# Optimization experiments

Measured on AMD Instinct MI355X. Metric: run time of the kernel, lower is better.

Reference implementation:

```python
import jax, jax.numpy as jnp
import numpy as np

B, S, H, D = 4, 128, 32, 128
T = 2048  # max_seq_len (cache length)
START_POS = 1024


def setup_inputs() -> dict:
    key = jax.random.key(0)
    ks = jax.random.split(key, 5)
    q = jax.random.normal(ks[0], (B, S, H, D), dtype=jnp.float32)
    k = jax.random.normal(ks[1], (B, S, H, D), dtype=jnp.float32)
    v = jax.random.normal(ks[2], (B, S, H, D), dtype=jnp.float32)
    k_cache = jax.random.normal(ks[3], (B, T, H, D), dtype=jnp.float32)
    v_cache = jax.random.normal(ks[4], (B, T, H, D), dtype=jnp.float32)
    return {"q": q, "k": k, "v": v, "k_cache": k_cache, "v_cache": v_cache,
            "input_pos": START_POS, "seq_len": S}


def reference(q, k, v, k_cache, v_cache, input_pos, seq_len):
    # Fused KV-cache append + causal SDPA (llama.sdpa_with_kv_cache semantics).
    # q/k/v: [B, S, H, D]; caches: [B, T, H, D]; input_pos = write offset.
    start = input_pos
    kc = jax.lax.dynamic_update_slice(k_cache, k, (0, start, 0, 0))
    vc = jax.lax.dynamic_update_slice(v_cache, v, (0, start, 0, 0))

    scale = 1.0 / jnp.sqrt(jnp.asarray(q.shape[-1], q.dtype))
    # scores: [B, H, S, T]
    scores = jnp.einsum('bshd,bthd->bhst', q, kc) * scale

    # causal mask relative to absolute positions: query i (global start+i)
    # attends to cache positions j <= start + i
    qpos = start + jnp.arange(seq_len)            # [S]
    kpos = jnp.arange(kc.shape[1])                # [T]
    mask = kpos[None, :] <= qpos[:, None]         # [S, T]
    neg = jnp.asarray(jnp.finfo(scores.dtype).min, scores.dtype)
    scores = jnp.where(mask[None, None], scores, neg)

    attn = jax.nn.softmax(scores, axis=-1)        # dropout = 0.0 (inference)
    out = jnp.einsum('bhst,bthd->bshd', attn, vc)  # [B, S, H, D]
    bsz = q.shape[0]
    return out.reshape(bsz, seq_len, -1)          # [B, S, H*D]
```

## Files before the change

### kernel.cpp

```cpp
#include <hip/hip_runtime.h>
#include <hip/hip_bf16.h>


typedef short bf16x8 __attribute__((ext_vector_type(8)));
typedef float f32x4  __attribute__((ext_vector_type(4)));

constexpr int B = 4, S = 128, H = 32, D = 128, T = 2048;
constexpr int KVBLK = 64;
constexpr int NS = 4;
constexpr float SCALE = 0.08838834764831845f;
constexpr float MNEG = -1e30f;

__device__ __forceinline__ short f2bf(float f) {
    return (short)__bfloat16_as_ushort(__float2bfloat16(f));
}
__device__ __forceinline__ unsigned pack_bf2(float a, float b) {
    return (unsigned)(unsigned short)__bfloat16_as_ushort(__float2bfloat16(a))
         | ((unsigned)__bfloat16_as_ushort(__float2bfloat16(b)) << 16);
}

__device__ __forceinline__ int kswz(int row, int cb) { return row * 256 + (cb ^ ((row & 7) << 4)); }
__device__ __forceinline__ int vswz(int row, int cb) { return 16384 + row * 128 + (cb ^ ((row & 7) << 4)); }

template<int MODE>
__global__ __launch_bounds__(512, 2) void sdpa_kernel(
    const float* __restrict__ qg, const float* __restrict__ kin,
    const float* __restrict__ vin, const float* __restrict__ kc,
    const float* __restrict__ vc, const int* __restrict__ ip,
    float* __restrict__ out, float* __restrict__ wsO, float2* __restrict__ wsML)
{
    __shared__ __align__(16) char smem[32768];

    const int start = ip[0];
    const int bh = blockIdx.x;
    const int b  = bh >> 5;
    const int h  = bh & 31;
    const int z  = (MODE == 1) ? blockIdx.z : 0;
    const int t  = threadIdx.x;
    const int w  = t >> 6;
    const int l  = t & 63;
    const int l16 = l & 15;
    const int lg  = l >> 4;
    const int qi  = w * 16 + l16;

    const float* qp = qg + (((size_t)b * S + qi) * H + h) * D;
    bf16x8 qfrag[4];
    #pragma unroll
    for (int ks = 0; ks < 4; ++ks) {
        const float* p = qp + ks * 32 + lg * 8;
        #pragma unroll
        for (int i = 0; i < 8; ++i) qfrag[ks][i] = f2bf(p[i]);
    }

    f32x4 oaccT[8];
    #pragma unroll
    for (int n = 0; n < 8; ++n) oaccT[n] = {0.f, 0.f, 0.f, 0.f};
    float m = MNEG, ssum = 0.f;

    const int kv_end = start + S;
    const int nt     = (kv_end + KVBLK - 1) / KVBLK;
    const int tstep  = (MODE == 1) ? NS : 1;
    const int t0     = (MODE == 1) ? z : 0;

    const int kr = t >> 5, c = t & 31;
    const int rb = t & 15, cb = t >> 4;

    auto kaddr = [&](int j) -> const float4* {
        return (j < start)
            ? (const float4*)(kc  + (((size_t)b * T + j) * H + h) * (size_t)D)
            : (const float4*)(kin + (((size_t)b * S + (j - start)) * H + h) * (size_t)D);
    };
    auto vaddr = [&](int j) -> const float4* {
        return (j < start)
            ? (const float4*)(vc  + (((size_t)b * T + j) * H + h) * (size_t)D)
            : (const float4*)(vin + (((size_t)b * S + (j - start)) * H + h) * (size_t)D);
    };

    for (int tile = t0; tile < nt; tile += tstep) {
        const int j0 = tile * KVBLK;

        #pragma unroll
        for (int g = 0; g < 2; ++g) {
            float4 kt[2];
            #pragma unroll
            for (int p = 0; p < 2; ++p) kt[p] = kaddr(j0 + (g * 2 + p) * 16 + kr)[c];
            #pragma unroll
            for (int p = 0; p < 2; ++p) {
                short4 k4b = { f2bf(kt[p].x), f2bf(kt[p].y), f2bf(kt[p].z), f2bf(kt[p].w) };
                *(short4*)(smem + kswz((g * 2 + p) * 16 + kr, c * 8)) = k4b;
            }
        }
        {
            float4 a[4];
            #pragma unroll
            for (int kk = 0; kk < 4; ++kk)
                a[kk] = vaddr(j0 + rb * 4 + kk)[cb];
            #pragma unroll
            for (int jj = 0; jj < 4; ++jj) {
                const int d = cb * 4 + jj;
                short4 wv = { f2bf(((const float*)&a[0])[jj]),
                              f2bf(((const float*)&a[1])[jj]),
                              f2bf(((const float*)&a[2])[jj]),
                              f2bf(((const float*)&a[3])[jj]) };
                *(short4*)(smem + vswz(d, rb * 8)) = wv;
            }
        }
        __syncthreads();

        if (j0 <= start + w * 16 + 15) {
            f32x4 sacc[4];
            #pragma unroll
            for (int n = 0; n < 4; ++n) sacc[n] = {0.f, 0.f, 0.f, 0.f};
            #pragma unroll
            for (int n = 0; n < 4; ++n) {
                #pragma unroll
                for (int ks = 0; ks < 4; ++ks) {
                    bf16x8 kfrag = *(const bf16x8*)(smem + kswz(n * 16 + l16, ks * 64 + lg * 16));
                    sacc[n] = __builtin_amdgcn_mfma_f32_16x16x32_bf16(
                        kfrag, qfrag[ks], sacc[n], 0, 0, 0);
                }
            }

            float pmax = MNEG;
            #pragma unroll
            for (int n = 0; n < 4; ++n) {
                #pragma unroll
                for (int j = 0; j < 4; ++j) {
                    const int kvj = j0 + n * 16 + lg * 4 + j;
                    float s = sacc[n][j] * SCALE;
                    if (kvj > start + qi) s = MNEG;
                    sacc[n][j] = s;
                    pmax = fmaxf(pmax, s);
                }
            }
            pmax = fmaxf(pmax, __shfl_xor(pmax, 16));
            pmax = fmaxf(pmax, __shfl_xor(pmax, 32));
            const float mnew = fmaxf(m, pmax);
            const float corr = __expf(m - mnew);
            m = mnew;

            float tsum = 0.f;
            unsigned plo[4], phi[4];
            #pragma unroll
            for (int n = 0; n < 4; ++n) {
                float p0 = __expf(sacc[n][0] - m);
                float p1 = __expf(sacc[n][1] - m);
                float p2 = __expf(sacc[n][2] - m);
                float p3 = __expf(sacc[n][3] - m);
                tsum += (p0 + p1) + (p2 + p3);
                plo[n] = pack_bf2(p0, p1);
                phi[n] = pack_bf2(p2, p3);
            }
            tsum += __shfl_xor(tsum, 16);
            tsum += __shfl_xor(tsum, 32);
            ssum = ssum * corr + tsum;
            #pragma unroll
            for (int n = 0; n < 8; ++n) {
                #pragma unroll
                for (int j = 0; j < 4; ++j) oaccT[n][j] *= corr;
            }

            const int sA = (((2 * lg)     & 3) << 4) | l16;
            const int sB = (((2 * lg + 1) & 3) << 4) | l16;
            const bool hi = (lg >= 2);
            bf16x8 pfragB[2];
            #pragma unroll
            for (int ks = 0; ks < 2; ++ks) {
                unsigned eA0 = __shfl(plo[2 * ks],     sA), eA1 = __shfl(phi[2 * ks],     sA);
                unsigned fA0 = __shfl(plo[2 * ks + 1], sA), fA1 = __shfl(phi[2 * ks + 1], sA);
                unsigned eB0 = __shfl(plo[2 * ks],     sB), eB1 = __shfl(phi[2 * ks],     sB);
                unsigned fB0 = __shfl(plo[2 * ks + 1], sB), fB1 = __shfl(phi[2 * ks + 1], sB);
                union { unsigned u[4]; bf16x8 v; } cv;
                cv.u[0] = hi ? fA0 : eA0;
                cv.u[1] = hi ? fA1 : eA1;
                cv.u[2] = hi ? fB0 : eB0;
                cv.u[3] = hi ? fB1 : eB1;
                pfragB[ks] = cv.v;
            }

            #pragma unroll
            for (int ks = 0; ks < 2; ++ks) {
                #pragma unroll
                for (int n = 0; n < 8; ++n) {
                    bf16x8 vfrag = *(const bf16x8*)(smem + vswz(n * 16 + l16, ks * 64 + lg * 16));
                    oaccT[n] = __builtin_amdgcn_mfma_f32_16x16x32_bf16(
                        vfrag, pfragB[ks], oaccT[n], 0, 0, 0);
                }
            }
        }
        __syncthreads();
    }

    float* scr = (float*)(smem + w * 4096);
    const float inv = (MODE == 0) ? 1.0f / ssum : 1.0f;
    #pragma unroll
    for (int half = 0; half < 2; ++half) {
        #pragma unroll
        for (int n2 = 0; n2 < 4; ++n2) {
            const int n = half * 4 + n2;
            #pragma unroll
            for (int j = 0; j < 4; ++j) {
                const int dl = n2 * 16 + lg * 4 + j;
                scr[l16 * 64 + (((dl & ~3) ^ ((l16 & 7) << 2)) | (dl & 3))] =
                    oaccT[n][j] * inv;
            }
        }
        asm volatile("s_waitcnt lgkmcnt(0)" ::: "memory");
        __builtin_amdgcn_sched_barrier(0);
        #pragma unroll
        for (int pass = 0; pass < 4; ++pass) {
            const int r  = pass * 4 + (l >> 4);
            const int d0 = (l & 15) * 4;
            f32x4 val = *(f32x4*)&scr[r * 64 + (d0 ^ ((r & 7) << 2))];
            const int qr = w * 16 + r;
            const int dc = half * 64 + d0;
            if (MODE == 0) {
                *(f32x4*)(out + ((size_t)b * S + qr) * (size_t)(H * D) + h * D + dc) = val;
            } else {
                *(f32x4*)(wsO + ((((size_t)z * B + b) * S + qr) * H + h) * (size_t)D + dc) = val;
            }
        }
        asm volatile("s_waitcnt lgkmcnt(0)" ::: "memory");
        __builtin_amdgcn_sched_barrier(0);
    }
    if (MODE == 1 && lg == 0)
        wsML[(((size_t)z * B + b) * S + qi) * H + h] = make_float2(m, ssum);
}

__global__ __launch_bounds__(256) void combine_kernel(
    const float* __restrict__ wsO, const float2* __restrict__ wsML,
    float* __restrict__ out)
{
    constexpr int R    = B * S * H;
    constexpr int TOT4 = R * D / 4;
    for (int i4 = blockIdx.x * 256 + threadIdx.x; i4 < TOT4;
         i4 += gridDim.x * 256) {
        const int row = i4 >> 5;
        float2 e[NS];
        float M = MNEG;
        #pragma unroll
        for (int cc = 0; cc < NS; ++cc) {
            e[cc] = wsML[(size_t)cc * R + row];
            M = fmaxf(M, e[cc].x);
        }
        float L = 0.f;
        float v0 = 0.f, v1 = 0.f, v2 = 0.f, v3 = 0.f;
        #pragma unroll
        for (int cc = 0; cc < NS; ++cc) {
            const float wgt = __expf(e[cc].x - M);
            L += e[cc].y * wgt;
            float4 tv = ((const float4*)wsO)[(size_t)cc * TOT4 + i4];
            v0 += tv.x * wgt; v1 += tv.y * wgt; v2 += tv.z * wgt; v3 += tv.w * wgt;
        }
        const float inv = 1.0f / L;
        ((float4*)out)[i4] = make_float4(v0 * inv, v1 * inv, v2 * inv, v3 * inv);
    }
}

extern "C" void kernel_launch(void* const* d_in, const int* in_sizes, int n_in,
                              void* d_out, int out_size, void* d_ws, size_t ws_size,
                              hipStream_t stream) {
    const float* q  = (const float*)d_in[0];
    const float* k  = (const float*)d_in[1];
    const float* v  = (const float*)d_in[2];
    const float* kc = (const float*)d_in[3];
    const float* vc = (const float*)d_in[4];
    const int*   ip = (const int*)d_in[5];
    float* out = (float*)d_out;

    const size_t nO  = (size_t)NS * B * S * H * D;
    const size_t nML = (size_t)NS * B * S * H;
    const size_t need = (nO + 2 * nML) * sizeof(float);

    if (ws_size >= need) {
        float*  wsO  = (float*)d_ws;
        float2* wsML = (float2*)(wsO + nO);
        sdpa_kernel<1><<<dim3(B * H, 1, NS), 512, 0, stream>>>(
            q, k, v, kc, vc, ip, out, wsO, wsML);
        combine_kernel<<<2048, 256, 0, stream>>>(wsO, wsML, out);
    } else {
        sdpa_kernel<0><<<dim3(B * H), 512, 0, stream>>>(
            q, k, v, kc, vc, ip, out, nullptr, nullptr);
    }
}
```

Measured before the change: 45.48 us.

## Double-buffer K/V tiles in LDS and prefetch next tile during compute

Doubles the shared-memory buffer to 64KB and restructures the KV loop into a software pipeline. The next tile's K and V global loads are issued before the current tile's QK and PV MFMAs, and the bf16 conversion and LDS stores go into the alternate buffer, so one barrier per iteration is dropped. The aim is to hide global-memory latency behind compute. The larger LDS footprint (64KB per block with launch_bounds(512,2)) may reduce occupancy, and the prefetched registers add pressure.

Result: slower. 52.73 us (+16.0%).

```diff
diff --git a/kernel.cpp b/kernel.cpp
--- a/kernel.cpp
+++ b/kernel.cpp
@@ -29,7 +29,7 @@
     const float* __restrict__ vc, const int* __restrict__ ip,
     float* __restrict__ out, float* __restrict__ wsO, float2* __restrict__ wsML)
 {
-    __shared__ __align__(16) char smem[32768];
+    __shared__ __align__(16) char smem[65536];
 
     const int start = ip[0];
     const int bh = blockIdx.x;
@@ -76,46 +76,57 @@
             : (const float4*)(vin + (((size_t)b * S + (j - start)) * H + h) * (size_t)D);
     };
 
+    {
+        const int j0 = t0 * KVBLK;
+        #pragma unroll
+        for (int p = 0; p < 4; ++p) {
+            float4 kt = kaddr(j0 + p * 16 + kr)[c];
+            short4 k4b = { f2bf(kt.x), f2bf(kt.y), f2bf(kt.z), f2bf(kt.w) };
+            *(short4*)(smem + kswz(p * 16 + kr, c * 8)) = k4b;
+        }
+        float4 a[4];
+        #pragma unroll
+        for (int kk = 0; kk < 4; ++kk) a[kk] = vaddr(j0 + rb * 4 + kk)[cb];
+        #pragma unroll
+        for (int jj = 0; jj < 4; ++jj) {
+            const int d = cb * 4 + jj;
+            short4 wv = { f2bf(((const float*)&a[0])[jj]),
+                          f2bf(((const float*)&a[1])[jj]),
+                          f2bf(((const float*)&a[2])[jj]),
+                          f2bf(((const float*)&a[3])[jj]) };
+            *(short4*)(smem + vswz(d, rb * 8)) = wv;
+        }
+    }
+    __syncthreads();
+
+    int cur = 0;
     for (int tile = t0; tile < nt; tile += tstep) {
-        const int j0 = tile * KVBLK;
-
-        #pragma unroll
-        for (int g = 0; g < 2; ++g) {
-            float4 kt[2];
-            #pragma unroll
-            for (int p = 0; p < 2; ++p) kt[p] = kaddr(j0 + (g * 2 + p) * 16 + kr)[c];
-            #pragma unroll
-            for (int p = 0; p < 2; ++p) {
-                short4 k4b = { f2bf(kt[p].x), f2bf(kt[p].y), f2bf(kt[p].z), f2bf(kt[p].w) };
-                *(short4*)(smem + kswz((g * 2 + p) * 16 + kr, c * 8)) = k4b;
-            }
-        }
-        {
-            float4 a[4];
-            #pragma unroll
-            for (int kk = 0; kk < 4; ++kk)
-                a[kk] = vaddr(j0 + rb * 4 + kk)[cb];
-            #pragma unroll
-            for (int jj = 0; jj < 4; ++jj) {
-                const int d = cb * 4 + jj;
-                short4 wv = { f2bf(((const float*)&a[0])[jj]),
-                              f2bf(((const float*)&a[1])[jj]),
-                              f2bf(((const float*)&a[2])[jj]),
-                              f2bf(((const float*)&a[3])[jj]) };
-                *(short4*)(smem + vswz(d, rb * 8)) = wv;
-            }
-        }
-        __syncthreads();
-
-        if (j0 <= start + w * 16 + 15) {
-            f32x4 sacc[4];
+        const int j0   = tile * KVBLK;
+        const int nxt  = tile + tstep;
+        const bool pre = (nxt < nt);
+        const int cb_cur = cur << 15;
+        const int cb_nxt = cb_cur ^ 32768;
+        const bool active = (j0 <= start + w * 16 + 15);
+
+        float4 kt[4];
+        if (pre) {
+            const int j0n = nxt * KVBLK;
+            #pragma unroll
+            for (int p = 0; p < 4; ++p) kt[p] = kaddr(j0n + p * 16 + kr)[c];
+        }
+        __builtin_amdgcn_sched_barrier(0);
+
+        f32x4 sacc[4];
+        unsigned plo[4], phi[4];
+        float corr;
+        if (active) {
             #pragma unroll
             for (int n = 0; n < 4; ++n) sacc[n] = {0.f, 0.f, 0.f, 0.f};
             #pragma unroll
             for (int n = 0; n < 4; ++n) {
                 #pragma unroll
                 for (int ks = 0; ks < 4; ++ks) {
-                    bf16x8 kfrag = *(const bf16x8*)(smem + kswz(n * 16 + l16, ks * 64 + lg * 16));
+                    bf16x8 kfrag = *(const bf16x8*)(smem + cb_cur + kswz(n * 16 + l16, ks * 64 + lg * 16));
                     sacc[n] = __builtin_amdgcn_mfma_f32_16x16x32_bf16(
                         kfrag, qfrag[ks], sacc[n], 0, 0, 0);
                 }
@@ -136,11 +147,10 @@
             pmax = fmaxf(pmax, __shfl_xor(pmax, 16));
             pmax = fmaxf(pmax, __shfl_xor(pmax, 32));
             const float mnew = fmaxf(m, pmax);
-            const float corr = __expf(m - mnew);
+            corr = __expf(m - mnew);
             m = mnew;
 
             float tsum = 0.f;
-            unsigned plo[4], phi[4];
             #pragma unroll
             for (int n = 0; n < 4; ++n) {
                 float p0 = __expf(sacc[n][0] - m);
@@ -159,7 +169,25 @@
                 #pragma unroll
                 for (int j = 0; j < 4; ++j) oaccT[n][j] *= corr;
             }
-
+        }
+
+        if (pre) {
+            #pragma unroll
+            for (int p = 0; p < 4; ++p) {
+                short4 k4b = { f2bf(kt[p].x), f2bf(kt[p].y), f2bf(kt[p].z), f2bf(kt[p].w) };
+                *(short4*)(smem + cb_nxt + kswz(p * 16 + kr, c * 8)) = k4b;
+            }
+        }
+
+        float4 av[4];
+        if (pre) {
+            const int j0n = nxt * KVBLK;
+            #pragma unroll
+            for (int kk = 0; kk < 4; ++kk) av[kk] = vaddr(j0n + rb * 4 + kk)[cb];
+        }
+        __builtin_amdgcn_sched_barrier(0);
+
+        if (active) {
             const int sA = (((2 * lg)     & 3) << 4) | l16;
             const int sB = (((2 * lg + 1) & 3) << 4) | l16;
             const bool hi = (lg >= 2);
@@ -182,13 +210,26 @@
             for (int ks = 0; ks < 2; ++ks) {
                 #pragma unroll
                 for (int n = 0; n < 8; ++n) {
-                    bf16x8 vfrag = *(const bf16x8*)(smem + vswz(n * 16 + l16, ks * 64 + lg * 16));
+                    bf16x8 vfrag = *(const bf16x8*)(smem + cb_cur + vswz(n * 16 + l16, ks * 64 + lg * 16));
                     oaccT[n] = __builtin_amdgcn_mfma_f32_16x16x32_bf16(
                         vfrag, pfragB[ks], oaccT[n], 0, 0, 0);
                 }
             }
         }
+
+        if (pre) {
+            #pragma unroll
+            for (int jj = 0; jj < 4; ++jj) {
+                const int d = cb * 4 + jj;
+                short4 wv = { f2bf(((const float*)&av[0])[jj]),
+                              f2bf(((const float*)&av[1])[jj]),
+                              f2bf(((const float*)&av[2])[jj]),
+                              f2bf(((const float*)&av[3])[jj]) };
+                *(short4*)(smem + cb_nxt + vswz(d, rb * 8)) = wv;
+            }
+        }
         __syncthreads();
+        cur ^= 1;
     }
 
     float* scr = (float*)(smem + w * 4096);
```

## Stage two KV tiles per barrier pair using doubled shared memory

Applied to the files above, without the earlier changes.

Each loop iteration now loads and converts two consecutive 64-row KV tiles into separate 32 KB halves of a 64 KB shared buffer, then computes both before the next barrier. This halves the number of __syncthreads rounds and puts more global loads in flight per phase. The split-K mode now distributes tile pairs across splits instead of single tiles, which changes the work balance. Doubling LDS use to 64 KB per block may reduce how many blocks fit per CU under launch_bounds(512,2).

Result: slower. 48.31 us (+6.2%).

```diff
diff --git a/kernel.cpp b/kernel.cpp
--- a/kernel.cpp
+++ b/kernel.cpp
@@ -29,7 +29,7 @@
     const float* __restrict__ vc, const int* __restrict__ ip,
     float* __restrict__ out, float* __restrict__ wsO, float2* __restrict__ wsML)
 {
-    __shared__ __align__(16) char smem[32768];
+    __shared__ __align__(16) char smem[65536];
 
     const int start = ip[0];
     const int bh = blockIdx.x;
@@ -57,10 +57,11 @@
     for (int n = 0; n < 8; ++n) oaccT[n] = {0.f, 0.f, 0.f, 0.f};
     float m = MNEG, ssum = 0.f;
 
-    const int kv_end = start + S;
-    const int nt     = (kv_end + KVBLK - 1) / KVBLK;
-    const int tstep  = (MODE == 1) ? NS : 1;
-    const int t0     = (MODE == 1) ? z : 0;
+    const int kv_end  = start + S;
+    const int nt      = (kv_end + KVBLK - 1) / KVBLK;
+    const int npairs  = (nt + 1) >> 1;
+    const int pstep   = (MODE == 1) ? NS : 1;
+    const int p0      = (MODE == 1) ? z : 0;
 
     const int kr = t >> 5, c = t & 31;
     const int rb = t & 15, cb = t >> 4;
@@ -76,38 +77,44 @@
             : (const float4*)(vin + (((size_t)b * S + (j - start)) * H + h) * (size_t)D);
     };
 
-    for (int tile = t0; tile < nt; tile += tstep) {
-        const int j0 = tile * KVBLK;
-
-        #pragma unroll
-        for (int g = 0; g < 2; ++g) {
-            float4 kt[2];
-            #pragma unroll
-            for (int p = 0; p < 2; ++p) kt[p] = kaddr(j0 + (g * 2 + p) * 16 + kr)[c];
-            #pragma unroll
-            for (int p = 0; p < 2; ++p) {
+    for (int pp = p0; pp < npairs; pp += pstep) {
+        #pragma unroll
+        for (int hh = 0; hh < 2; ++hh) {
+            const int tile = 2 * pp + hh;
+            if (tile >= nt) break;
+            const int j0   = tile * KVBLK;
+            const int hoff = hh << 15;
+            float4 kt[4];
+            #pragma unroll
+            for (int p = 0; p < 4; ++p) kt[p] = kaddr(j0 + p * 16 + kr)[c];
+            float4 av[4];
+            #pragma unroll
+            for (int kk = 0; kk < 4; ++kk) av[kk] = vaddr(j0 + rb * 4 + kk)[cb];
+            #pragma unroll
+            for (int p = 0; p < 4; ++p) {
                 short4 k4b = { f2bf(kt[p].x), f2bf(kt[p].y), f2bf(kt[p].z), f2bf(kt[p].w) };
-                *(short4*)(smem + kswz((g * 2 + p) * 16 + kr, c * 8)) = k4b;
-            }
-        }
-        {
-            float4 a[4];
-            #pragma unroll
-            for (int kk = 0; kk < 4; ++kk)
-                a[kk] = vaddr(j0 + rb * 4 + kk)[cb];
+                *(short4*)(smem + hoff + kswz(p * 16 + kr, c * 8)) = k4b;
+            }
             #pragma unroll
             for (int jj = 0; jj < 4; ++jj) {
                 const int d = cb * 4 + jj;
-                short4 wv = { f2bf(((const float*)&a[0])[jj]),
-                              f2bf(((const float*)&a[1])[jj]),
-                              f2bf(((const float*)&a[2])[jj]),
-                              f2bf(((const float*)&a[3])[jj]) };
-                *(short4*)(smem + vswz(d, rb * 8)) = wv;
+                short4 wv = { f2bf(((const float*)&av[0])[jj]),
+                              f2bf(((const float*)&av[1])[jj]),
+                              f2bf(((const float*)&av[2])[jj]),
+                              f2bf(((const float*)&av[3])[jj]) };
+                *(short4*)(smem + hoff + vswz(d, rb * 8)) = wv;
             }
         }
         __syncthreads();
 
-        if (j0 <= start + w * 16 + 15) {
+        #pragma unroll
+        for (int hh = 0; hh < 2; ++hh) {
+            const int tile = 2 * pp + hh;
+            if (tile >= nt) break;
+            const int j0   = tile * KVBLK;
+            const int hoff = hh << 15;
+            if (j0 > start + w * 16 + 15) continue;
+
             f32x4 sacc[4];
             #pragma unroll
             for (int n = 0; n < 4; ++n) sacc[n] = {0.f, 0.f, 0.f, 0.f};
@@ -115,7 +122,7 @@
             for (int n = 0; n < 4; ++n) {
                 #pragma unroll
                 for (int ks = 0; ks < 4; ++ks) {
-                    bf16x8 kfrag = *(const bf16x8*)(smem + kswz(n * 16 + l16, ks * 64 + lg * 16));
+                    bf16x8 kfrag = *(const bf16x8*)(smem + hoff + kswz(n * 16 + l16, ks * 64 + lg * 16));
                     sacc[n] = __builtin_amdgcn_mfma_f32_16x16x32_bf16(
                         kfrag, qfrag[ks], sacc[n], 0, 0, 0);
                 }
@@ -143,13 +150,13 @@
             unsigned plo[4], phi[4];
             #pragma unroll
             for (int n = 0; n < 4; ++n) {
-                float p0 = __expf(sacc[n][0] - m);
-                float p1 = __expf(sacc[n][1] - m);
-                float p2 = __expf(sacc[n][2] - m);
-                float p3 = __expf(sacc[n][3] - m);
-                tsum += (p0 + p1) + (p2 + p3);
-                plo[n] = pack_bf2(p0, p1);
-                phi[n] = pack_bf2(p2, p3);
+                float q0e = __expf(sacc[n][0] - m);
+                float q1e = __expf(sacc[n][1] - m);
+                float q2e = __expf(sacc[n][2] - m);
+                float q3e = __expf(sacc[n][3] - m);
+                tsum += (q0e + q1e) + (q2e + q3e);
+                plo[n] = pack_bf2(q0e, q1e);
+                phi[n] = pack_bf2(q2e, q3e);
             }
             tsum += __shfl_xor(tsum, 16);
             tsum += __shfl_xor(tsum, 32);
@@ -182,7 +189,7 @@
             for (int ks = 0; ks < 2; ++ks) {
                 #pragma unroll
                 for (int n = 0; n < 8; ++n) {
-                    bf16x8 vfrag = *(const bf16x8*)(smem + vswz(n * 16 + l16, ks * 64 + lg * 16));
+                    bf16x8 vfrag = *(const bf16x8*)(smem + hoff + vswz(n * 16 + l16, ks * 64 + lg * 16));
                     oaccT[n] = __builtin_amdgcn_mfma_f32_16x16x32_bf16(
                         vfrag, pfragB[ks], oaccT[n], 0, 0, 0);
                 }
```
